# Performance work log

Hardware: AMD Instinct MI355X
Metric: run time of the kernel (lower is better)

Reference implementation:

```python
import math
import jax, jax.numpy as jnp
import numpy as np

DIM = 256
B = 32
M = 2048
N = 2048


def setup_inputs() -> dict:
    key = jax.random.key(0)
    k1, k2, k3, k4 = jax.random.split(key, 4)
    query = jax.random.normal(k1, (B, DIM, M), dtype=jnp.float32)
    key_t = jax.random.normal(k2, (B, DIM, N), dtype=jnp.float32)
    value = jax.random.normal(k3, (B, DIM, N), dtype=jnp.float32)
    # orthogonal random projection via QR, as in the torch __init__
    proj = np.asarray(jax.random.normal(k4, (DIM, DIM), dtype=jnp.float32))
    orth_proj, _ = np.linalg.qr(proj)
    orth_proj = jnp.asarray(orth_proj, dtype=jnp.float32)
    return {"query": query, "key": key_t, "value": value, "orth_proj": orth_proj}


def reference(query, key, value, orth_proj):
    dim = orth_proj.shape[0]
    q = query / math.sqrt(dim)
    # kernel feature maps: relu(W^T x), channels-first layout b c m
    phi_q = jax.nn.relu(jnp.einsum('bcm,ce->bem', q, orth_proj))
    phi_k = jax.nn.relu(jnp.einsum('bcn,ce->ben', key, orth_proj))
    phi_k_rowsum = phi_k.sum(-1)                         # [b, e]
    scale = jnp.einsum('bem,be->bm', phi_q, phi_k_rowsum)  # [b, m]
    scale = 1.0 / (scale + 1e-8)
    phi_q = phi_q * scale[:, None, :]                    # [b, e, m]
    kv = jnp.einsum('ben,bdn->bed', phi_k, value)        # [b, e, d]
    out = jnp.einsum('bem,bed->bdm', phi_q, kv)          # [b, d, m]
    return out
```

## Files before the change

### kernel.cpp

```cpp
#include <hip/hip_runtime.h>

#define DIMC 256
#define BSZ  32
#define MDIM 2048
#define NDIM 2048

#define KVP_STRIDE ((size_t)BSZ * DIMC * DIMC)

typedef __attribute__((ext_vector_type(8))) short bf16x8;
typedef __attribute__((ext_vector_type(4))) float f32x4;

static __device__ __forceinline__ unsigned short f2bf(float x) {
  unsigned int u = __float_as_uint(x);
  u += 0x7fffu + ((u >> 16) & 1u);
  return (unsigned short)(u >> 16);
}
static __device__ __forceinline__ float bf2f(unsigned short h) {
  return __uint_as_float(((unsigned int)h) << 16);
}
static __device__ __forceinline__ unsigned int cvt_pk_bf16(float lo, float hi) {
  unsigned int r;
  asm("v_cvt_pk_bf16_f32 %0, %1, %2" : "=v"(r) : "v"(lo), "v"(hi));
  return r;
}

__global__ __launch_bounds__(256) void prep_kernel(
    const float* __restrict__ W, unsigned short* __restrict__ Wt,
    float* __restrict__ rowsum) {
  const int e = blockIdx.x, c = threadIdx.x;
  Wt[e * 256 + c] = f2bf(W[c * 256 + e]);
  if (e < 32) rowsum[e * 256 + c] = 0.f;
}

__global__ __launch_bounds__(256) void phiq_kernel(
    const float* __restrict__ query, const unsigned short* __restrict__ Wt,
    unsigned short* __restrict__ phi_q) {
  __shared__ unsigned short As[128 * 40];
  __shared__ unsigned short Bs[128 * 40];
  const int b = blockIdx.z;
  const int m0 = blockIdx.x * 128;
  const int e0 = blockIdx.y * 128;
  const int t = threadIdx.x;
  const int lane = t & 63, wave = t >> 6;
  const int wr = wave >> 1, wc = wave & 1;
  const int q = lane >> 4, l15 = lane & 15;
  const float* qb = query + (size_t)b * DIMC * MDIM;
  f32x4 acc[4][4];
#pragma unroll
  for (int i = 0; i < 4; ++i)
#pragma unroll
    for (int j = 0; j < 4; ++j) acc[i][j] = (f32x4){0.f, 0.f, 0.f, 0.f};

  const int brow = t >> 2, bc8 = (t & 3) << 3;
  const int midx = t & 127, ch = (t >> 7) << 4;

  for (int k0 = 0; k0 < DIMC; k0 += 32) {
    __syncthreads();
    {
      const float* src = qb + (size_t)(k0 + ch) * MDIM + m0 + midx;
      float v[16];
#pragma unroll
      for (int i = 0; i < 16; ++i) v[i] = src[(size_t)i * MDIM];
      unsigned int w[8];
#pragma unroll
      for (int i = 0; i < 8; ++i) w[i] = cvt_pk_bf16(v[2 * i], v[2 * i + 1]);
      *(uint4*)&As[midx * 40 + ch] = *(const uint4*)&w[0];
      *(uint4*)&As[midx * 40 + ch + 8] = *(const uint4*)&w[4];
    }
    {
      uint4 v0 = *(const uint4*)(Wt + (size_t)(e0 + brow) * 256 + k0 + bc8);
      uint4 v1 = *(const uint4*)(Wt + (size_t)(e0 + brow + 64) * 256 + k0 + bc8);
      *(uint4*)&Bs[brow * 40 + bc8] = v0;
      *(uint4*)&Bs[(brow + 64) * 40 + bc8] = v1;
    }
    __syncthreads();
    bf16x8 a[4], bv[4];
#pragma unroll
    for (int i = 0; i < 4; ++i)
      a[i] = *(const bf16x8*)&As[(wr * 64 + i * 16 + l15) * 40 + q * 8];
#pragma unroll
    for (int j = 0; j < 4; ++j)
      bv[j] = *(const bf16x8*)&Bs[(wc * 64 + j * 16 + l15) * 40 + q * 8];
#pragma unroll
    for (int i = 0; i < 4; ++i)
#pragma unroll
      for (int j = 0; j < 4; ++j)
        acc[i][j] =
            __builtin_amdgcn_mfma_f32_16x16x32_bf16(a[i], bv[j], acc[i][j], 0, 0, 0);
  }
  unsigned short* dst = phi_q + (size_t)b * MDIM * DIMC;
#pragma unroll
  for (int i = 0; i < 4; ++i)
#pragma unroll
    for (int j = 0; j < 4; ++j) {
      const int e = e0 + wc * 64 + j * 16 + l15;
#pragma unroll
      for (int r = 0; r < 4; ++r) {
        const int m = m0 + wr * 64 + i * 16 + q * 4 + r;
        float v = acc[i][j][r];
        v = v > 0.f ? v * 0.0625f : 0.f;
        dst[(size_t)m * DIMC + e] = f2bf(v);
      }
    }
}

__global__ __launch_bounds__(256) void phik_kernel(
    const float* __restrict__ key, const unsigned short* __restrict__ Wt,
    unsigned short* __restrict__ phi_k, float* __restrict__ rowsum) {
  __shared__ unsigned short As[128 * 40];
  __shared__ unsigned short Bs[128 * 40];
  const int b = blockIdx.z;
  const int n0 = blockIdx.x * 128;
  const int e0 = blockIdx.y * 128;
  const int t = threadIdx.x;
  const int lane = t & 63, wave = t >> 6;
  const int wr = wave >> 1, wc = wave & 1;
  const int q = lane >> 4, l15 = lane & 15;
  const float* keyb = key + (size_t)b * DIMC * NDIM;
  f32x4 acc[4][4];
#pragma unroll
  for (int i = 0; i < 4; ++i)
#pragma unroll
    for (int j = 0; j < 4; ++j) acc[i][j] = (f32x4){0.f, 0.f, 0.f, 0.f};

  const int arow = t >> 2, ac8 = (t & 3) << 3;
  const int nidx = t & 127, ch = (t >> 7) << 4;

  for (int k0 = 0; k0 < DIMC; k0 += 32) {
    __syncthreads();
    {
      uint4 v0 = *(const uint4*)(Wt + (size_t)(e0 + arow) * 256 + k0 + ac8);
      uint4 v1 = *(const uint4*)(Wt + (size_t)(e0 + arow + 64) * 256 + k0 + ac8);
      *(uint4*)&As[arow * 40 + ac8] = v0;
      *(uint4*)&As[(arow + 64) * 40 + ac8] = v1;
    }
    {
      const float* src = keyb + (size_t)(k0 + ch) * NDIM + n0 + nidx;
      float v[16];
#pragma unroll
      for (int i = 0; i < 16; ++i) v[i] = src[(size_t)i * NDIM];
      unsigned int w[8];
#pragma unroll
      for (int i = 0; i < 8; ++i) w[i] = cvt_pk_bf16(v[2 * i], v[2 * i + 1]);
      *(uint4*)&Bs[nidx * 40 + ch] = *(const uint4*)&w[0];
      *(uint4*)&Bs[nidx * 40 + ch + 8] = *(const uint4*)&w[4];
    }
    __syncthreads();
    bf16x8 a[4], bv[4];
#pragma unroll
    for (int i = 0; i < 4; ++i)
      a[i] = *(const bf16x8*)&As[(wr * 64 + i * 16 + l15) * 40 + q * 8];
#pragma unroll
    for (int j = 0; j < 4; ++j)
      bv[j] = *(const bf16x8*)&Bs[(wc * 64 + j * 16 + l15) * 40 + q * 8];
#pragma unroll
    for (int i = 0; i < 4; ++i)
#pragma unroll
      for (int j = 0; j < 4; ++j)
        acc[i][j] =
            __builtin_amdgcn_mfma_f32_16x16x32_bf16(a[i], bv[j], acc[i][j], 0, 0, 0);
  }
  unsigned short* dst = phi_k + (size_t)b * DIMC * NDIM;
#pragma unroll
  for (int i = 0; i < 4; ++i)
#pragma unroll
    for (int r = 0; r < 4; ++r) {
      const int e = e0 + wr * 64 + i * 16 + q * 4 + r;
      float s = 0.f;
#pragma unroll
      for (int j = 0; j < 4; ++j) {
        float v = acc[i][j][r];
        v = v > 0.f ? v : 0.f;
        const int n = n0 + wc * 64 + j * 16 + l15;
        dst[(size_t)e * NDIM + n] = f2bf(v);
        s += v;
      }
#pragma unroll
      for (int m = 1; m < 16; m <<= 1) s += __shfl_xor(s, m, 64);
      if (l15 == 0) atomicAdd(&rowsum[b * DIMC + e], s);
    }
}

__global__ __launch_bounds__(256) void kv_kernel(
    const float* __restrict__ value, const unsigned short* __restrict__ phi_k,
    unsigned short* __restrict__ kvp) {
  __shared__ unsigned short As[128 * 72];
  __shared__ unsigned short Bs[128 * 72];
  const int b = blockIdx.z >> 1, ks = blockIdx.z & 1;
  const int d0 = blockIdx.x * 128, e0 = blockIdx.y * 128;
  const int t = threadIdx.x;
  const int lane = t & 63, wave = t >> 6;
  const int wr = wave >> 1, wc = wave & 1;
  const int q = lane >> 4, l15 = lane & 15;
  f32x4 acc[4][4];
#pragma unroll
  for (int i = 0; i < 4; ++i)
#pragma unroll
    for (int j = 0; j < 4; ++j) acc[i][j] = (f32x4){0.f, 0.f, 0.f, 0.f};

  const int row = t >> 2;
  const int c4 = (t & 3) << 2;
  const int c8 = (t & 3) << 3;

  const float* asrc0 = value + ((size_t)b * DIMC + d0 + row) * NDIM;
  const float* asrc1 = asrc0 + (size_t)64 * NDIM;
  const unsigned short* bsrc0 = phi_k + ((size_t)b * DIMC + e0 + row) * NDIM;
  const unsigned short* bsrc1 = bsrc0 + (size_t)64 * NDIM;

  const int nbeg = ks * (NDIM / 2);
  for (int n0 = nbeg; n0 < nbeg + NDIM / 2; n0 += 64) {
    __syncthreads();
#pragma unroll
    for (int i = 0; i < 4; ++i) {
      float4 f0 = *(const float4*)(asrc0 + n0 + c4 + i * 16);
      float4 f1 = *(const float4*)(asrc1 + n0 + c4 + i * 16);
      uint2 w0, w1;
      w0.x = cvt_pk_bf16(f0.x, f0.y); w0.y = cvt_pk_bf16(f0.z, f0.w);
      w1.x = cvt_pk_bf16(f1.x, f1.y); w1.y = cvt_pk_bf16(f1.z, f1.w);
      *(uint2*)&As[row * 72 + c4 + i * 16] = w0;
      *(uint2*)&As[(row + 64) * 72 + c4 + i * 16] = w1;
    }
#pragma unroll
    for (int i = 0; i < 2; ++i) {
      uint4 p0 = *(const uint4*)(bsrc0 + n0 + c8 + i * 32);
      uint4 p1 = *(const uint4*)(bsrc1 + n0 + c8 + i * 32);
      *(uint4*)&Bs[row * 72 + c8 + i * 32] = p0;
      *(uint4*)&Bs[(row + 64) * 72 + c8 + i * 32] = p1;
    }
    __syncthreads();
#pragma unroll
    for (int kk = 0; kk < 64; kk += 32) {
      bf16x8 a[4], bv[4];
#pragma unroll
      for (int i = 0; i < 4; ++i)
        a[i] = *(const bf16x8*)&As[(wr * 64 + i * 16 + l15) * 72 + kk + q * 8];
#pragma unroll
      for (int j = 0; j < 4; ++j)
        bv[j] = *(const bf16x8*)&Bs[(wc * 64 + j * 16 + l15) * 72 + kk + q * 8];
#pragma unroll
      for (int i = 0; i < 4; ++i)
#pragma unroll
        for (int j = 0; j < 4; ++j)
          acc[i][j] = __builtin_amdgcn_mfma_f32_16x16x32_bf16(a[i], bv[j],
                                                              acc[i][j], 0, 0, 0);
    }
  }
  unsigned short* dst = kvp + (size_t)ks * KVP_STRIDE + (size_t)b * DIMC * DIMC;
#pragma unroll
  for (int i = 0; i < 4; ++i)
#pragma unroll
    for (int j = 0; j < 4; ++j) {
      const int e = e0 + wc * 64 + j * 16 + l15;
#pragma unroll
      for (int r = 0; r < 4; ++r) {
        const int d = d0 + wr * 64 + i * 16 + q * 4 + r;
        dst[(size_t)d * DIMC + e] = f2bf(acc[i][j][r]);
      }
    }
}

__global__ __launch_bounds__(256) void out_kernel(
    const unsigned short* __restrict__ kvp,
    const unsigned short* __restrict__ phi_q,
    const float* __restrict__ rowsum, float* __restrict__ out) {
  __shared__ unsigned short As[128 * 40];
  __shared__ unsigned short Bs[128 * 40];
  __shared__ float rs_lds[256];
  __shared__ float red[512];
  __shared__ float scl[128];
  const int b = blockIdx.z;
  const int m0 = blockIdx.x * 128;
  const int d0 = blockIdx.y * 128;
  const int t = threadIdx.x;
  const int lane = t & 63, wave = t >> 6;
  const int wr = wave >> 1, wc = wave & 1;
  const int q = lane >> 4, l15 = lane & 15;

  rs_lds[t] = rowsum[b * DIMC + t];

  f32x4 acc[4][4];
#pragma unroll
  for (int i = 0; i < 4; ++i)
#pragma unroll
    for (int j = 0; j < 4; ++j) acc[i][j] = (f32x4){0.f, 0.f, 0.f, 0.f};

  const int row = t >> 2, c8 = (t & 3) << 3;
  const unsigned short* a0 = kvp + ((size_t)b * DIMC + d0 + row) * DIMC + c8;
  const unsigned short* a1 = a0 + (size_t)64 * DIMC;
  const unsigned short* bsrc0 = phi_q + ((size_t)b * MDIM + m0 + row) * DIMC + c8;
  const unsigned short* bsrc1 = bsrc0 + (size_t)64 * DIMC;
  float sA = 0.f, sB = 0.f;

  for (int k0 = 0; k0 < DIMC; k0 += 32) {
    __syncthreads();
    {
      float pa8[8], pb8[8];
      uint4 pa0 = *(const uint4*)(a0 + k0);
      uint4 pb0 = *(const uint4*)(a1 + k0);
      uint4 pa1 = *(const uint4*)(a0 + KVP_STRIDE + k0);
      uint4 pb1 = *(const uint4*)(a1 + KVP_STRIDE + k0);
      const unsigned short* ua0 = (const unsigned short*)&pa0;
      const unsigned short* ub0 = (const unsigned short*)&pb0;
      const unsigned short* ua1 = (const unsigned short*)&pa1;
      const unsigned short* ub1 = (const unsigned short*)&pb1;
#pragma unroll
      for (int j = 0; j < 8; ++j) {
        pa8[j] = bf2f(ua0[j]) + bf2f(ua1[j]);
        pb8[j] = bf2f(ub0[j]) + bf2f(ub1[j]);
      }
      unsigned int wa[4], wb[4];
#pragma unroll
      for (int j = 0; j < 4; ++j) {
        wa[j] = cvt_pk_bf16(pa8[2 * j], pa8[2 * j + 1]);
        wb[j] = cvt_pk_bf16(pb8[2 * j], pb8[2 * j + 1]);
      }
      *(uint4*)&As[row * 40 + c8] = *(const uint4*)wa;
      *(uint4*)&As[(row + 64) * 40 + c8] = *(const uint4*)wb;
    }
    {
      uint4 q0 = *(const uint4*)(bsrc0 + k0);
      uint4 q1 = *(const uint4*)(bsrc1 + k0);
      *(uint4*)&Bs[row * 40 + c8] = q0;
      *(uint4*)&Bs[(row + 64) * 40 + c8] = q1;
      const unsigned short* u0 = (const unsigned short*)&q0;
      const unsigned short* u1 = (const unsigned short*)&q1;
#pragma unroll
      for (int j = 0; j < 8; ++j) {
        const float r = rs_lds[k0 + c8 + j];
        sA += bf2f(u0[j]) * r;
        sB += bf2f(u1[j]) * r;
      }
    }
    __syncthreads();
    bf16x8 a[4], bv[4];
#pragma unroll
    for (int i = 0; i < 4; ++i)
      a[i] = *(const bf16x8*)&As[(wr * 64 + i * 16 + l15) * 40 + q * 8];
#pragma unroll
    for (int j = 0; j < 4; ++j)
      bv[j] = *(const bf16x8*)&Bs[(wc * 64 + j * 16 + l15) * 40 + q * 8];
#pragma unroll
    for (int i = 0; i < 4; ++i)
#pragma unroll
      for (int j = 0; j < 4; ++j)
        acc[i][j] =
            __builtin_amdgcn_mfma_f32_16x16x32_bf16(a[i], bv[j], acc[i][j], 0, 0, 0);
  }
  __syncthreads();
  red[row * 4 + (t & 3)] = sA;
  red[(row + 64) * 4 + (t & 3)] = sB;
  __syncthreads();
  if (t < 128) {
    float s = red[t * 4] + red[t * 4 + 1] + red[t * 4 + 2] + red[t * 4 + 3];
    scl[t] = 1.f / (s + 1e-8f);
  }
  __syncthreads();

  float* ob = out + (size_t)b * DIMC * MDIM;
#pragma unroll
  for (int j = 0; j < 4; ++j) {
    const int ml = wc * 64 + j * 16 + l15;
    const int m = m0 + ml;
    const float sc = scl[ml];
#pragma unroll
    for (int i = 0; i < 4; ++i) {
#pragma unroll
      for (int r = 0; r < 4; ++r) {
        const int d = d0 + wr * 64 + i * 16 + q * 4 + r;
        ob[(size_t)d * MDIM + m] = acc[i][j][r] * sc;
      }
    }
  }
}

extern "C" void kernel_launch(void* const* d_in, const int* in_sizes, int n_in,
                              void* d_out, int out_size, void* d_ws, size_t ws_size,
                              hipStream_t stream) {
  const float* query = (const float*)d_in[0];
  const float* key   = (const float*)d_in[1];
  const float* value = (const float*)d_in[2];
  const float* W     = (const float*)d_in[3];
  float* out = (float*)d_out;

  unsigned short* Wt    = (unsigned short*)d_ws;
  unsigned short* phi_q = Wt + 65536;
  unsigned short* phi_k = phi_q + (size_t)BSZ * MDIM * DIMC;
  unsigned short* kvp   = phi_k + (size_t)BSZ * DIMC * NDIM;
  float* rowsum = (float*)(kvp + 2 * KVP_STRIDE);

  hipLaunchKernelGGL(prep_kernel, dim3(256), dim3(256), 0, stream, W, Wt, rowsum);
  hipLaunchKernelGGL(phiq_kernel, dim3(MDIM / 128, DIMC / 128, BSZ), dim3(256),
                     0, stream, query, Wt, phi_q);
  hipLaunchKernelGGL(phik_kernel, dim3(NDIM / 128, DIMC / 128, BSZ), dim3(256),
                     0, stream, key, Wt, phi_k, rowsum);
  hipLaunchKernelGGL(kv_kernel, dim3(DIMC / 128, DIMC / 128, BSZ * 2), dim3(256),
                     0, stream, value, phi_k, kvp);
  hipLaunchKernelGGL(out_kernel, dim3(MDIM / 128, DIMC / 128, BSZ), dim3(256),
                     0, stream, kvp, phi_q, rowsum, out);
}
```

Baseline: 301.0 us.

## Raise kv split-K to eight with separate reduction kernel; prefetch GEMM tiles in registers

The kv GEMM now splits the N reduction into up to eight chunks instead of two, sized to fit the workspace, so that grid is larger. A new kvred kernel sums the bf16 partials into the first slot, which removes the partial-sum logic from out_kernel. The phiq, phik and out kernels now load the next K tile into registers while the current tile is in MFMA, add an occupancy hint, and move the barrier to the end of each iteration. The cost is an extra launch, more partial-buffer traffic, and extra rounding from summing bf16 partials.

```diff
diff --git a/kernel.cpp b/kernel.cpp
--- a/kernel.cpp
+++ b/kernel.cpp
@@ -32,7 +32,7 @@
   if (e < 32) rowsum[e * 256 + c] = 0.f;
 }
 
-__global__ __launch_bounds__(256) void phiq_kernel(
+__global__ __launch_bounds__(256, 4) void phiq_kernel(
     const float* __restrict__ query, const unsigned short* __restrict__ Wt,
     unsigned short* __restrict__ phi_q) {
   __shared__ unsigned short As[128 * 40];
@@ -53,27 +53,35 @@
 
   const int brow = t >> 2, bc8 = (t & 3) << 3;
   const int midx = t & 127, ch = (t >> 7) << 4;
-
-  for (int k0 = 0; k0 < DIMC; k0 += 32) {
-    __syncthreads();
+  const float* src0 = qb + (size_t)ch * MDIM + m0 + midx;
+  const unsigned short* wt0 = Wt + (size_t)(e0 + brow) * 256 + bc8;
+  const unsigned short* wt1 = Wt + (size_t)(e0 + brow + 64) * 256 + bc8;
+
+  float v[16];
+#pragma unroll
+  for (int i = 0; i < 16; ++i) v[i] = src0[(size_t)i * MDIM];
+  uint4 w0 = *(const uint4*)wt0;
+  uint4 w1 = *(const uint4*)wt1;
+
+  for (int it = 0; it < 8; ++it) {
+    const int k0 = it * 32;
     {
-      const float* src = qb + (size_t)(k0 + ch) * MDIM + m0 + midx;
-      float v[16];
+      unsigned int wpk[8];
+#pragma unroll
+      for (int i = 0; i < 8; ++i) wpk[i] = cvt_pk_bf16(v[2 * i], v[2 * i + 1]);
+      *(uint4*)&As[midx * 40 + ch] = *(const uint4*)&wpk[0];
+      *(uint4*)&As[midx * 40 + ch + 8] = *(const uint4*)&wpk[4];
+      *(uint4*)&Bs[brow * 40 + bc8] = w0;
+      *(uint4*)&Bs[(brow + 64) * 40 + bc8] = w1;
+    }
+    __syncthreads();
+    if (it < 7) {
+      const float* src = src0 + (size_t)(k0 + 32) * MDIM;
 #pragma unroll
       for (int i = 0; i < 16; ++i) v[i] = src[(size_t)i * MDIM];
-      unsigned int w[8];
-#pragma unroll
-      for (int i = 0; i < 8; ++i) w[i] = cvt_pk_bf16(v[2 * i], v[2 * i + 1]);
-      *(uint4*)&As[midx * 40 + ch] = *(const uint4*)&w[0];
-      *(uint4*)&As[midx * 40 + ch + 8] = *(const uint4*)&w[4];
-    }
-    {
-      uint4 v0 = *(const uint4*)(Wt + (size_t)(e0 + brow) * 256 + k0 + bc8);
-      uint4 v1 = *(const uint4*)(Wt + (size_t)(e0 + brow + 64) * 256 + k0 + bc8);
-      *(uint4*)&Bs[brow * 40 + bc8] = v0;
-      *(uint4*)&Bs[(brow + 64) * 40 + bc8] = v1;
-    }
-    __syncthreads();
+      w0 = *(const uint4*)(wt0 + k0 + 32);
+      w1 = *(const uint4*)(wt1 + k0 + 32);
+    }
     bf16x8 a[4], bv[4];
 #pragma unroll
     for (int i = 0; i < 4; ++i)
@@ -87,6 +95,7 @@
       for (int j = 0; j < 4; ++j)
         acc[i][j] =
             __builtin_amdgcn_mfma_f32_16x16x32_bf16(a[i], bv[j], acc[i][j], 0, 0, 0);
+    __syncthreads();
   }
   unsigned short* dst = phi_q + (size_t)b * MDIM * DIMC;
 #pragma unroll
@@ -97,14 +106,14 @@
 #pragma unroll
       for (int r = 0; r < 4; ++r) {
         const int m = m0 + wr * 64 + i * 16 + q * 4 + r;
-        float v = acc[i][j][r];
-        v = v > 0.f ? v * 0.0625f : 0.f;
-        dst[(size_t)m * DIMC + e] = f2bf(v);
+        float vv = acc[i][j][r];
+        vv = vv > 0.f ? vv * 0.0625f : 0.f;
+        dst[(size_t)m * DIMC + e] = f2bf(vv);
       }
     }
 }
 
-__global__ __launch_bounds__(256) void phik_kernel(
+__global__ __launch_bounds__(256, 4) void phik_kernel(
     const float* __restrict__ key, const unsigned short* __restrict__ Wt,
     unsigned short* __restrict__ phi_k, float* __restrict__ rowsum) {
   __shared__ unsigned short As[128 * 40];
@@ -125,27 +134,35 @@
 
   const int arow = t >> 2, ac8 = (t & 3) << 3;
   const int nidx = t & 127, ch = (t >> 7) << 4;
-
-  for (int k0 = 0; k0 < DIMC; k0 += 32) {
-    __syncthreads();
+  const float* src0 = keyb + (size_t)ch * NDIM + n0 + nidx;
+  const unsigned short* wt0 = Wt + (size_t)(e0 + arow) * 256 + ac8;
+  const unsigned short* wt1 = Wt + (size_t)(e0 + arow + 64) * 256 + ac8;
+
+  float v[16];
+#pragma unroll
+  for (int i = 0; i < 16; ++i) v[i] = src0[(size_t)i * NDIM];
+  uint4 w0 = *(const uint4*)wt0;
+  uint4 w1 = *(const uint4*)wt1;
+
+  for (int it = 0; it < 8; ++it) {
+    const int k0 = it * 32;
     {
-      uint4 v0 = *(const uint4*)(Wt + (size_t)(e0 + arow) * 256 + k0 + ac8);
-      uint4 v1 = *(const uint4*)(Wt + (size_t)(e0 + arow + 64) * 256 + k0 + ac8);
-      *(uint4*)&As[arow * 40 + ac8] = v0;
-      *(uint4*)&As[(arow + 64) * 40 + ac8] = v1;
-    }
-    {
-      const float* src = keyb + (size_t)(k0 + ch) * NDIM + n0 + nidx;
-      float v[16];
+      unsigned int wpk[8];
+#pragma unroll
+      for (int i = 0; i < 8; ++i) wpk[i] = cvt_pk_bf16(v[2 * i], v[2 * i + 1]);
+      *(uint4*)&Bs[nidx * 40 + ch] = *(const uint4*)&wpk[0];
+      *(uint4*)&Bs[nidx * 40 + ch + 8] = *(const uint4*)&wpk[4];
+      *(uint4*)&As[arow * 40 + ac8] = w0;
+      *(uint4*)&As[(arow + 64) * 40 + ac8] = w1;
+    }
+    __syncthreads();
+    if (it < 7) {
+      const float* src = src0 + (size_t)(k0 + 32) * NDIM;
 #pragma unroll
       for (int i = 0; i < 16; ++i) v[i] = src[(size_t)i * NDIM];
-      unsigned int w[8];
-#pragma unroll
-      for (int i = 0; i < 8; ++i) w[i] = cvt_pk_bf16(v[2 * i], v[2 * i + 1]);
-      *(uint4*)&Bs[nidx * 40 + ch] = *(const uint4*)&w[0];
-      *(uint4*)&Bs[nidx * 40 + ch + 8] = *(const uint4*)&w[4];
-    }
-    __syncthreads();
+      w0 = *(const uint4*)(wt0 + k0 + 32);
+      w1 = *(const uint4*)(wt1 + k0 + 32);
+    }
     bf16x8 a[4], bv[4];
 #pragma unroll
     for (int i = 0; i < 4; ++i)
@@ -159,6 +176,7 @@
       for (int j = 0; j < 4; ++j)
         acc[i][j] =
             __builtin_amdgcn_mfma_f32_16x16x32_bf16(a[i], bv[j], acc[i][j], 0, 0, 0);
+    __syncthreads();
   }
   unsigned short* dst = phi_k + (size_t)b * DIMC * NDIM;
 #pragma unroll
@@ -169,11 +187,11 @@
       float s = 0.f;
 #pragma unroll
       for (int j = 0; j < 4; ++j) {
-        float v = acc[i][j][r];
-        v = v > 0.f ? v : 0.f;
+        float vv = acc[i][j][r];
+        vv = vv > 0.f ? vv : 0.f;
         const int n = n0 + wc * 64 + j * 16 + l15;
-        dst[(size_t)e * NDIM + n] = f2bf(v);
-        s += v;
+        dst[(size_t)e * NDIM + n] = f2bf(vv);
+        s += vv;
       }
 #pragma unroll
       for (int m = 1; m < 16; m <<= 1) s += __shfl_xor(s, m, 64);
@@ -183,10 +201,10 @@
 
 __global__ __launch_bounds__(256) void kv_kernel(
     const float* __restrict__ value, const unsigned short* __restrict__ phi_k,
-    unsigned short* __restrict__ kvp) {
+    unsigned short* __restrict__ kvp, int kshift) {
   __shared__ unsigned short As[128 * 72];
   __shared__ unsigned short Bs[128 * 72];
-  const int b = blockIdx.z >> 1, ks = blockIdx.z & 1;
+  const int b = blockIdx.z >> kshift, ks = blockIdx.z & ((1 << kshift) - 1);
   const int d0 = blockIdx.x * 128, e0 = blockIdx.y * 128;
   const int t = threadIdx.x;
   const int lane = t & 63, wave = t >> 6;
@@ -207,8 +225,9 @@
   const unsigned short* bsrc0 = phi_k + ((size_t)b * DIMC + e0 + row) * NDIM;
   const unsigned short* bsrc1 = bsrc0 + (size_t)64 * NDIM;
 
-  const int nbeg = ks * (NDIM / 2);
-  for (int n0 = nbeg; n0 < nbeg + NDIM / 2; n0 += 64) {
+  const int nchunk = NDIM >> kshift;
+  const int nbeg = ks * nchunk;
+  for (int n0 = nbeg; n0 < nbeg + nchunk; n0 += 64) {
     __syncthreads();
 #pragma unroll
     for (int i = 0; i < 4; ++i) {
@@ -259,8 +278,26 @@
     }
 }
 
-__global__ __launch_bounds__(256) void out_kernel(
-    const unsigned short* __restrict__ kvp,
+__global__ __launch_bounds__(256) void kvred_kernel(
+    unsigned short* __restrict__ kvp, int KS) {
+  const size_t idx8 = ((size_t)blockIdx.x * 256 + threadIdx.x) * 8;
+  float s[8];
+#pragma unroll
+  for (int j = 0; j < 8; ++j) s[j] = 0.f;
+  for (int p = 0; p < KS; ++p) {
+    uint4 v = *(const uint4*)(kvp + (size_t)p * KVP_STRIDE + idx8);
+    const unsigned short* u = (const unsigned short*)&v;
+#pragma unroll
+    for (int j = 0; j < 8; ++j) s[j] += bf2f(u[j]);
+  }
+  unsigned int w[4];
+#pragma unroll
+  for (int j = 0; j < 4; ++j) w[j] = cvt_pk_bf16(s[2 * j], s[2 * j + 1]);
+  *(uint4*)(kvp + idx8) = *(const uint4*)w;
+}
+
+__global__ __launch_bounds__(256, 4) void out_kernel(
+    const unsigned short* __restrict__ kv,
     const unsigned short* __restrict__ phi_q,
     const float* __restrict__ rowsum, float* __restrict__ out) {
   __shared__ unsigned short As[128 * 40];
@@ -285,45 +322,26 @@
     for (int j = 0; j < 4; ++j) acc[i][j] = (f32x4){0.f, 0.f, 0.f, 0.f};
 
   const int row = t >> 2, c8 = (t & 3) << 3;
-  const unsigned short* a0 = kvp + ((size_t)b * DIMC + d0 + row) * DIMC + c8;
+  const unsigned short* a0 = kv + ((size_t)b * DIMC + d0 + row) * DIMC + c8;
   const unsigned short* a1 = a0 + (size_t)64 * DIMC;
   const unsigned short* bsrc0 = phi_q + ((size_t)b * MDIM + m0 + row) * DIMC + c8;
   const unsigned short* bsrc1 = bsrc0 + (size_t)64 * DIMC;
   float sA = 0.f, sB = 0.f;
 
-  for (int k0 = 0; k0 < DIMC; k0 += 32) {
-    __syncthreads();
+  uint4 pa0 = *(const uint4*)a0;
+  uint4 pa1 = *(const uint4*)a1;
+  uint4 pq0 = *(const uint4*)bsrc0;
+  uint4 pq1 = *(const uint4*)bsrc1;
+
+  for (int it = 0; it < 8; ++it) {
+    const int k0 = it * 32;
     {
-      float pa8[8], pb8[8];
-      uint4 pa0 = *(const uint4*)(a0 + k0);
-      uint4 pb0 = *(const uint4*)(a1 + k0);
-      uint4 pa1 = *(const uint4*)(a0 + KVP_STRIDE + k0);
-      uint4 pb1 = *(const uint4*)(a1 + KVP_STRIDE + k0);
-      const unsigned short* ua0 = (const unsigned short*)&pa0;
-      const unsigned short* ub0 = (const unsigned short*)&pb0;
-      const unsigned short* ua1 = (const unsigned short*)&pa1;
-      const unsigned short* ub1 = (const unsigned short*)&pb1;
-#pragma unroll
-      for (int j = 0; j < 8; ++j) {
-        pa8[j] = bf2f(ua0[j]) + bf2f(ua1[j]);
-        pb8[j] = bf2f(ub0[j]) + bf2f(ub1[j]);
-      }
-      unsigned int wa[4], wb[4];
-#pragma unroll
-      for (int j = 0; j < 4; ++j) {
-        wa[j] = cvt_pk_bf16(pa8[2 * j], pa8[2 * j + 1]);
-        wb[j] = cvt_pk_bf16(pb8[2 * j], pb8[2 * j + 1]);
-      }
-      *(uint4*)&As[row * 40 + c8] = *(const uint4*)wa;
-      *(uint4*)&As[(row + 64) * 40 + c8] = *(const uint4*)wb;
-    }
-    {
-      uint4 q0 = *(const uint4*)(bsrc0 + k0);
-      uint4 q1 = *(const uint4*)(bsrc1 + k0);
-      *(uint4*)&Bs[row * 40 + c8] = q0;
-      *(uint4*)&Bs[(row + 64) * 40 + c8] = q1;
-      const unsigned short* u0 = (const unsigned short*)&q0;
-      const unsigned short* u1 = (const unsigned short*)&q1;
+      *(uint4*)&As[row * 40 + c8] = pa0;
+      *(uint4*)&As[(row + 64) * 40 + c8] = pa1;
+      *(uint4*)&Bs[row * 40 + c8] = pq0;
+      *(uint4*)&Bs[(row + 64) * 40 + c8] = pq1;
+      const unsigned short* u0 = (const unsigned short*)&pq0;
+      const unsigned short* u1 = (const unsigned short*)&pq1;
 #pragma unroll
       for (int j = 0; j < 8; ++j) {
         const float r = rs_lds[k0 + c8 + j];
@@ -332,6 +350,12 @@
       }
     }
     __syncthreads();
+    if (it < 7) {
+      pa0 = *(const uint4*)(a0 + k0 + 32);
+      pa1 = *(const uint4*)(a1 + k0 + 32);
+      pq0 = *(const uint4*)(bsrc0 + k0 + 32);
+      pq1 = *(const uint4*)(bsrc1 + k0 + 32);
+    }
     bf16x8 a[4], bv[4];
 #pragma unroll
     for (int i = 0; i < 4; ++i)
@@ -345,8 +369,8 @@
       for (int j = 0; j < 4; ++j)
         acc[i][j] =
             __builtin_amdgcn_mfma_f32_16x16x32_bf16(a[i], bv[j], acc[i][j], 0, 0, 0);
-  }
-  __syncthreads();
+    __syncthreads();
+  }
   red[row * 4 + (t & 3)] = sA;
   red[(row + 64) * 4 + (t & 3)] = sB;
   __syncthreads();
@@ -386,15 +410,27 @@
   unsigned short* phi_q = Wt + 65536;
   unsigned short* phi_k = phi_q + (size_t)BSZ * MDIM * DIMC;
   unsigned short* kvp   = phi_k + (size_t)BSZ * DIMC * NDIM;
-  float* rowsum = (float*)(kvp + 2 * KVP_STRIDE);
+
+  const size_t base_shorts =
+      65536 + (size_t)BSZ * MDIM * DIMC + (size_t)BSZ * DIMC * NDIM;
+  int KS = 8, kshift = 3;
+  while (KS > 1 &&
+         (base_shorts + (size_t)KS * KVP_STRIDE) * 2 + (size_t)BSZ * DIMC * 4 >
+             ws_size) {
+    KS >>= 1;
+    kshift -= 1;
+  }
+  float* rowsum = (float*)(kvp + (size_t)KS * KVP_STRIDE);
 
   hipLaunchKernelGGL(prep_kernel, dim3(256), dim3(256), 0, stream, W, Wt, rowsum);
   hipLaunchKernelGGL(phiq_kernel, dim3(MDIM / 128, DIMC / 128, BSZ), dim3(256),
                      0, stream, query, Wt, phi_q);
   hipLaunchKernelGGL(phik_kernel, dim3(NDIM / 128, DIMC / 128, BSZ), dim3(256),
                      0, stream, key, Wt, phi_k, rowsum);
-  hipLaunchKernelGGL(kv_kernel, dim3(DIMC / 128, DIMC / 128, BSZ * 2), dim3(256),
-                     0, stream, value, phi_k, kvp);
+  hipLaunchKernelGGL(kv_kernel, dim3(DIMC / 128, DIMC / 128, BSZ << kshift),
+                     dim3(256), 0, stream, value, phi_k, kvp, kshift);
+  if (KS > 1)
+    hipLaunchKernelGGL(kvred_kernel, dim3(1024), dim3(256), 0, stream, kvp, KS);
   hipLaunchKernelGGL(out_kernel, dim3(MDIM / 128, DIMC / 128, BSZ), dim3(256),
                      0, stream, kvp, phi_q, rowsum, out);
 }
```

Measured after the change: 310.3 us. 1.03x slower.
